# Optimization experiments

Measured on AMD Instinct MI355X. Metric: run time of the kernel, lower is better.

Reference implementation:

```python
import jax, jax.numpy as jnp
import numpy as np

B, T, D = 64, 256, 300
H = 256            # each_state = state_size // 2
G = 4 * H          # gate dim = state_size * 2
N = 8              # num_bases
M, KQ = 64, 64     # meta_dim, key_query_size
V = 10000          # meta vocab


def setup_inputs() -> dict:
    key = jax.random.key(0)
    ks = jax.random.split(key, 16)
    s = 0.05
    return {
        'x': jax.random.normal(ks[0], (B, T, D), jnp.float32),
        'length': jax.random.randint(ks[1], (B,), 1, T + 1),
        'user_idx': jax.random.randint(ks[2], (B,), 0, V),
        'item_idx': jax.random.randint(ks[3], (B,), 0, V),
        'user_emb': jax.random.normal(ks[4], (V, M), jnp.float32) * s,
        'item_emb': jax.random.normal(ks[5], (V, M), jnp.float32) * s,
        'W1': jax.random.normal(ks[6], (2 * M, KQ), jnp.float32) * s,
        'b1': jax.random.normal(ks[7], (KQ,), jnp.float32) * s,
        'W2': jax.random.normal(ks[8], (KQ, N), jnp.float32) * s,
        'Wih': jax.random.normal(ks[9], (N, G, D), jnp.float32) * s,
        'Whh': jax.random.normal(ks[10], (N, G, H), jnp.float32) * s,
        'bias': jax.random.normal(ks[11], (N, G), jnp.float32) * s,
        'Wih_r': jax.random.normal(ks[12], (N, G, D), jnp.float32) * s,
        'Whh_r': jax.random.normal(ks[13], (N, G, H), jnp.float32) * s,
        'bias_r': jax.random.normal(ks[14], (N, G), jnp.float32) * s,
    }


def _run_dir(xs, mask, Wi, Wh, bb):
    # xs: [T,B,D], mask: [T,B] True where state forced to zero
    b, h = xs.shape[1], Wh.shape[2]
    h0 = jnp.zeros((b, h), xs.dtype)

    def step(carry, inp):
        hx, cx = carry
        xt, m = inp
        gates = (jnp.einsum('bgi,bi->bg', Wi, xt)
                 + jnp.einsum('bgh,bh->bg', Wh, hx) + bb)
        ig, fg, gg, og = jnp.split(gates, 4, axis=1)
        cy = jax.nn.sigmoid(fg) * cx + jax.nn.sigmoid(ig) * jnp.tanh(gg)
        hy = jax.nn.sigmoid(og) * jnp.tanh(cy)
        cy = jnp.where(m[:, None], 0.0, cy)
        hy = jnp.where(m[:, None], 0.0, hy)
        return (hy, cy), hy

    _, hs = jax.lax.scan(step, (h0, h0), (xs, mask))
    return hs  # [T,B,H]


def reference(x, length, user_idx, item_idx, user_emb, item_emb,
              W1, b1, W2, Wih, Whh, bias, Wih_r, Whh_r, bias_r):
    # basis mixing coefficients per sample
    q = jnp.concatenate([user_emb[user_idx], item_emb[item_idx]], axis=1)  # [B,2M]
    c = jax.nn.softmax(jnp.tanh(q @ W1 + b1) @ W2, axis=1)                 # [B,N]
    mix = lambda w: jnp.einsum('bn,n...->b...', c, w)

    Bc, Tc = x.shape[0], x.shape[1]
    t = jnp.arange(Tc)
    mask_f = t[:, None] >= length[None, :]            # length - 1 < i
    mask_r = (Tc - t)[:, None] > length[None, :]      # maxlength - i > length

    xs = jnp.swapaxes(x, 0, 1)                        # [T,B,D]
    h_f = _run_dir(xs, mask_f, mix(Wih), mix(Whh), mix(bias))
    h_r = _run_dir(xs[::-1], mask_r, mix(Wih_r), mix(Whh_r), mix(bias_r))
    h_r = h_r[::-1]                                   # un-reverse in time
    return jnp.concatenate([h_f, h_r], axis=-1).swapaxes(0, 1)  # [B,T,2H]
```

## Files before the change

kernel.cpp:

```cpp
#include <hip/hip_runtime.h>

#define B_ 64
#define T_ 256
#define D_ 300
#define DP_ 320
#define H_ 256
#define G_ 1024
#define N_ 8

typedef unsigned int u32;
typedef unsigned short u16;
typedef __attribute__((ext_vector_type(8))) short short8;
typedef __attribute__((ext_vector_type(4))) float f32x4;
typedef __attribute__((ext_vector_type(4))) u32 u32x4;
typedef __attribute__((ext_vector_type(2))) u32 u32x2;
typedef _Float16 h2 __attribute__((ext_vector_type(2)));
typedef __fp16 fp16x2 __attribute__((ext_vector_type(2)));

__device__ __forceinline__ u16 f2bf(float f){
  union {float f; u32 u;} v; v.f = f;
  u32 r = (v.u + 0x7fffu + ((v.u>>16)&1u)) >> 16;
  return (u16)r;
}
__device__ __forceinline__ float bflo(u32 u){
  union {u32 u; float f;} v; v.u = u<<16; return v.f;
}
__device__ __forceinline__ float bfhi(u32 u){
  union {u32 u; float f;} v; v.u = u & 0xffff0000u; return v.f;
}
__device__ __forceinline__ float sigm(float x){ return 1.0f/(1.0f+__expf(-x)); }
__device__ __forceinline__ float tanh_(float x){ return 2.0f/(1.0f+__expf(-2.0f*x)) - 1.0f; }

__device__ __forceinline__ float fdot2(u32 a, u32 b, float c){
  union { u32 u; h2 h; } ua, ub; ua.u = a; ub.u = b;
#if __has_builtin(__builtin_amdgcn_fdot2)
  return __builtin_amdgcn_fdot2(ua.h, ub.h, c, false);
#else
  return c + (float)ua.h.x*(float)ub.h.x + (float)ua.h.y*(float)ub.h.y;
#endif
}
__device__ __forceinline__ u32 pkf16(float a, float b){
  union { fp16x2 h; u32 u; } v; v.h = __builtin_amdgcn_cvt_pkrtz(a, b); return v.u;
}

__global__ void __launch_bounds__(64) k_coef(
    const int* __restrict__ uidx, const int* __restrict__ iidx,
    const float* __restrict__ uemb, const float* __restrict__ iemb,
    const float* __restrict__ W1, const float* __restrict__ b1,
    const float* __restrict__ W2, float* __restrict__ coef)
{
  __shared__ float q[128];
  __shared__ float hid[64];
  __shared__ float lg[8];
  int b = blockIdx.x, t = threadIdx.x;
  int u = uidx[b], it = iidx[b];
  q[t]      = uemb[(size_t)u*64 + t];
  q[64 + t] = iemb[(size_t)it*64 + t];
  __syncthreads();
  float s = b1[t];
  for (int j = 0; j < 128; ++j) s = fmaf(q[j], W1[j*64 + t], s);
  hid[t] = tanhf(s);
  __syncthreads();
  if (t < 8) {
    float s2 = 0.f;
    for (int j = 0; j < 64; ++j) s2 = fmaf(hid[j], W2[j*8 + t], s2);
    lg[t] = s2;
  }
  __syncthreads();
  if (t == 0) {
    float mx = lg[0];
    for (int n = 1; n < 8; ++n) mx = fmaxf(mx, lg[n]);
    float e[8], den = 0.f;
    for (int n = 0; n < 8; ++n){ e[n] = __expf(lg[n]-mx); den += e[n]; }
    for (int n = 0; n < 8; ++n) coef[b*8+n] = e[n]/den;
  }
}

__global__ void __launch_bounds__(256) k_mix_whh(
    const float* __restrict__ Whh_f, const float* __restrict__ Whh_r,
    const float* __restrict__ bias_f, const float* __restrict__ bias_r,
    const float* __restrict__ coef, u32* __restrict__ blob, float* __restrict__ bias_m)
{
  int gblk = blockIdx.x;
  int dir  = blockIdx.y;
  int tid  = threadIdx.x;
  const float* Wsel = dir ? Whh_r : Whh_f;
  const float* bsel = dir ? bias_r : bias_f;
  __shared__ float bs[N_][8][H_];
  for (int v = 0; v < 64; ++v){
    int i = v*256 + tid;
    int n = i >> 11, gl = (i >> 8) & 7, c = i & 255;
    bs[n][gl][c] = Wsel[((size_t)n*G_ + gblk*8 + gl)*H_ + c];
  }
  __syncthreads();
  int t2l = tid & 7, ii = tid >> 3;
  int tid2 = gblk*8 + t2l;
  int gg = tid2 >> 2, q = tid2 & 3;
  int cidx = ii >> 2, e = ii & 3;
  int p = q*32 + ((cidx + 2*q)&7)*4 + e;
  int glbase = gg*4 - gblk*8;
  float bw0[4][8], bw1[4][8];
  #pragma unroll
  for (int l = 0; l < 4; ++l)
    #pragma unroll
    for (int n = 0; n < 8; ++n){
      bw0[l][n] = bs[n][glbase + l][2*p];
      bw1[l][n] = bs[n][glbase + l][2*p + 1];
    }
  for (int b = 0; b < B_; ++b){
    float c8[8];
    #pragma unroll
    for (int n = 0; n < 8; ++n) c8[n] = coef[b*8+n];
    u32x4 ov;
    #pragma unroll
    for (int l = 0; l < 4; ++l){
      float w0 = 0.f, w1 = 0.f;
      #pragma unroll
      for (int n = 0; n < 8; ++n){ w0 = fmaf(c8[n], bw0[l][n], w0); w1 = fmaf(c8[n], bw1[l][n], w1); }
      ov[l] = pkf16(w0, w1);
    }
    size_t chain = (size_t)(dir*B_ + b);
    *(u32x4*)(blob + ((chain*32 + ii)*1024 + tid2)*4) = ov;
    if (tid < 8){
      float bb = 0.f;
      #pragma unroll
      for (int n = 0; n < 8; ++n) bb = fmaf(c8[n], bsel[n*G_ + gblk*8 + tid], bb);
      bias_m[chain*G_ + gblk*8 + tid] = bb;
    }
  }
}

__global__ void __launch_bounds__(256) k_mix_wi(
    const float* __restrict__ Wih_f, const float* __restrict__ Wih_r,
    const float* __restrict__ coef, u32* __restrict__ WimU)
{
  int gblk = blockIdx.x;
  int dir  = blockIdx.y;
  int tid  = threadIdx.x;
  const float* Wsel = dir ? Wih_r : Wih_f;
  __shared__ float bs[N_][8][D_];
  for (int v = 0; v < 75; ++v){
    int i = v*256 + tid;
    int n = i/2400, rem = i%2400, gl = rem/300, c = rem%300;
    bs[n][gl][c] = Wsel[((size_t)n*G_ + gblk*8 + gl)*D_ + c];
  }
  __syncthreads();
  float bw[5][2][8];
  int rowv[5], cpv[5];
  #pragma unroll
  for (int v = 0; v < 5; ++v){
    int idx = v*256 + tid;
    int row = idx/160, cp = idx%160;
    rowv[v] = row; cpv[v] = cp;
    #pragma unroll
    for (int n = 0; n < 8; ++n){
      bw[v][0][n] = (cp < 150) ? bs[n][row][2*cp]   : 0.f;
      bw[v][1][n] = (cp < 150) ? bs[n][row][2*cp+1] : 0.f;
    }
  }
  for (int b = 0; b < B_; ++b){
    float c8[8];
    #pragma unroll
    for (int n = 0; n < 8; ++n) c8[n] = coef[b*8+n];
    #pragma unroll
    for (int v = 0; v < 5; ++v){
      float w0 = 0.f, w1 = 0.f;
      #pragma unroll
      for (int n = 0; n < 8; ++n){ w0 = fmaf(c8[n], bw[v][0][n], w0); w1 = fmaf(c8[n], bw[v][1][n], w1); }
      WimU[(((size_t)(dir*B_+b)*G_ + gblk*8 + rowv[v])*160) + cpv[v]] = (u32)f2bf(w0) | ((u32)f2bf(w1) << 16);
    }
  }
}

__global__ void __launch_bounds__(256) k_xpad(const float* __restrict__ x, u32* __restrict__ xpadU)
{
  int o = blockIdx.x*256 + threadIdx.x;
  int bt = o/160, cp = o%160;
  float v0 = (cp < 150) ? x[(size_t)bt*D_ + 2*cp]   : 0.f;
  float v1 = (cp < 150) ? x[(size_t)bt*D_ + 2*cp+1] : 0.f;
  xpadU[o] = (u32)f2bf(v0) | ((u32)f2bf(v1) << 16);
}

__global__ void __launch_bounds__(256,2) k_gemm(
    const u16* __restrict__ xpad, const u16* __restrict__ Wim,
    const float* __restrict__ bias_m, u16* __restrict__ xproj)
{
  int bx = blockIdx.x;
  int b  = blockIdx.y, dir = blockIdx.z;
  int tt = bx >> 3, tg = bx & 7;
  int tid = threadIdx.x;
  int wid = tid >> 6, lane = tid & 63;
  int wr = wid >> 1, wc = wid & 1;
  __shared__ u16 As[128][72];
  __shared__ u16 Bs[128][72];
  const u16* Ap = xpad + ((size_t)b*T_ + tt*128)*DP_;
  const u16* Bp = Wim + (((size_t)dir*B_ + b)*G_ + tg*128)*DP_;
  f32x4 acc[4][4];
  #pragma unroll
  for (int i = 0; i < 4; ++i)
    #pragma unroll
    for (int j = 0; j < 4; ++j) acc[i][j] = (f32x4){0.f,0.f,0.f,0.f};
  for (int kt = 0; kt < 5; ++kt){
    int k0 = kt*64;
    #pragma unroll
    for (int i = 0; i < 4; ++i){
      int ci = i*256 + tid;
      int row = ci >> 3, cc = (ci & 7)*8;
      *(u32x4*)&As[row][cc] = *(const u32x4*)(Ap + (size_t)row*DP_ + k0 + cc);
      *(u32x4*)&Bs[row][cc] = *(const u32x4*)(Bp + (size_t)row*DP_ + k0 + cc);
    }
    __syncthreads();
    #pragma unroll
    for (int kk = 0; kk < 2; ++kk){
      short8 af[4], bfr[4];
      #pragma unroll
      for (int mi = 0; mi < 4; ++mi) af[mi]  = *(const short8*)&As[wr*64 + mi*16 + (lane&15)][kk*32 + (lane>>4)*8];
      #pragma unroll
      for (int ni = 0; ni < 4; ++ni) bfr[ni] = *(const short8*)&Bs[wc*64 + ni*16 + (lane&15)][kk*32 + (lane>>4)*8];
      #pragma unroll
      for (int mi = 0; mi < 4; ++mi)
        #pragma unroll
        for (int ni = 0; ni < 4; ++ni)
          acc[mi][ni] = __builtin_amdgcn_mfma_f32_16x16x32_bf16(af[mi], bfr[ni], acc[mi][ni], 0,0,0);
    }
    __syncthreads();
  }
  int r4 = (lane >> 4)*4, cg = lane & 15;
  const float* bmp = bias_m + (size_t)(dir*B_ + b)*G_;
  #pragma unroll
  for (int ni = 0; ni < 4; ++ni){
    int g = tg*128 + wc*64 + ni*16 + cg;
    float bsv = bmp[g];
    #pragma unroll
    for (int mi = 0; mi < 4; ++mi)
      #pragma unroll
      for (int j = 0; j < 4; ++j){
        int t = tt*128 + wr*64 + mi*16 + r4 + j;
        xproj[(((size_t)dir*B_ + b)*T_ + t)*G_ + g] = f2bf(acc[mi][ni][j] + bsv);
      }
  }
}

__global__ void __launch_bounds__(1024) k_rec(
    const u32* __restrict__ blob, const u32* __restrict__ xprojU,
    const int* __restrict__ length, float* __restrict__ out)
{
  int chain = blockIdx.x;
  int dir = chain >> 6, b = chain & 63;
  int tid = threadIdx.x;
  int gg = tid >> 2, q = tid & 3;
  __shared__ u32 wlds[8][1024][4];
  __shared__ __align__(16) float gates4[256][4];
  __shared__ __align__(16) u16 hp16[256];
  const u32* hp32 = (const u32*)hp16;

  u32 w[96];
  const u32* bp = blob + (size_t)chain*32*1024*4;
  #pragma unroll
  for (int ii = 0; ii < 24; ++ii){
    u32x4 v = *(const u32x4*)(bp + ((size_t)ii*1024 + tid)*4);
    w[4*ii] = v.x; w[4*ii+1] = v.y; w[4*ii+2] = v.z; w[4*ii+3] = v.w;
  }
  #pragma unroll
  for (int ii = 24; ii < 32; ++ii){
    u32x4 v = *(const u32x4*)(bp + ((size_t)ii*1024 + tid)*4);
    *(u32x4*)&wlds[ii-24][tid][0] = v;
  }
  if (tid < 256) hp16[tid] = 0;
  int len = length[b];
  const u32* xp = xprojU + (size_t)chain*T_*512;
  float* outp = out + (size_t)b*T_*512 + dir*H_;
  float cst = 0.f;
  __syncthreads();

  for (int step = 0; step < len; ++step){
    int t = dir ? (len-1-step) : step;
    u32 xv0 = 0, xv1 = 0;
    if (q == 0){
      u32x2 xv = *(const u32x2*)(xp + (size_t)t*512 + 2*gg);
      xv0 = xv.x; xv1 = xv.y;
    }
    float a0 = 0.f, a1 = 0.f, a2 = 0.f, a3 = 0.f;
    #pragma unroll
    for (int cidx = 0; cidx < 8; ++cidx){
      int c4 = (cidx + 2*q) & 7;
      u32x4 hq = *(const u32x4*)&hp32[q*32 + c4*4];
      if (cidx < 6){
        #pragma unroll
        for (int e = 0; e < 4; ++e){
          u32 hv = hq[e];
          a0 = fdot2(w[cidx*16 + e*4 + 0], hv, a0);
          a1 = fdot2(w[cidx*16 + e*4 + 1], hv, a1);
          a2 = fdot2(w[cidx*16 + e*4 + 2], hv, a2);
          a3 = fdot2(w[cidx*16 + e*4 + 3], hv, a3);
        }
      } else {
        #pragma unroll
        for (int e = 0; e < 4; ++e){
          u32x4 wv = *(const u32x4*)&wlds[cidx*4 + e - 24][tid][0];
          u32 hv = hq[e];
          a0 = fdot2(wv.x, hv, a0);
          a1 = fdot2(wv.y, hv, a1);
          a2 = fdot2(wv.z, hv, a2);
          a3 = fdot2(wv.w, hv, a3);
        }
      }
    }
    a0 += __shfl_xor(a0, 1); a0 += __shfl_xor(a0, 2);
    a1 += __shfl_xor(a1, 1); a1 += __shfl_xor(a1, 2);
    a2 += __shfl_xor(a2, 1); a2 += __shfl_xor(a2, 2);
    a3 += __shfl_xor(a3, 1); a3 += __shfl_xor(a3, 2);
    if (q == 0){
      a0 += bflo(xv0); a1 += bfhi(xv0); a2 += bflo(xv1); a3 += bfhi(xv1);
      f32x4 g4; g4.x = a0; g4.y = a1; g4.z = a2; g4.w = a3;
      *(f32x4*)&gates4[gg][0] = g4;
    }
    __syncthreads();
    if (tid < 256){
      const float* gf = &gates4[0][0];
      float ig = gf[tid],       fg = gf[256 + tid];
      float g_ = gf[512 + tid], og = gf[768 + tid];
      float i_ = sigm(ig), f_ = sigm(fg), gt = tanh_(g_), o_ = sigm(og);
      float cn = fmaf(f_, cst, i_*gt);
      float hy = o_ * tanh_(cn);
      cst = cn;
      ((u16*)hp16)[tid] = (u16)(pkf16(hy, hy) & 0xffffu);
      outp[(size_t)t*512 + tid] = hy;
    }
    __syncthreads();
  }
}

extern "C" void kernel_launch(void* const* d_in, const int* in_sizes, int n_in,
                              void* d_out, int out_size, void* d_ws, size_t ws_size,
                              hipStream_t stream)
{
  const float* x      = (const float*)d_in[0];
  const int*   length = (const int*)d_in[1];
  const int*   uidx   = (const int*)d_in[2];
  const int*   iidx   = (const int*)d_in[3];
  const float* uemb   = (const float*)d_in[4];
  const float* iemb   = (const float*)d_in[5];
  const float* W1     = (const float*)d_in[6];
  const float* b1     = (const float*)d_in[7];
  const float* W2     = (const float*)d_in[8];
  const float* Wih    = (const float*)d_in[9];
  const float* Whh    = (const float*)d_in[10];
  const float* bias   = (const float*)d_in[11];
  const float* Wih_r  = (const float*)d_in[12];
  const float* Whh_r  = (const float*)d_in[13];
  const float* bias_r = (const float*)d_in[14];
  float* out = (float*)d_out;
  char* ws = (char*)d_ws;

  float* coef   = (float*)(ws + 0);
  float* bias_m = (float*)(ws + 2048);
  u32*   blob   = (u32*)  (ws + 526336);
  u16*   Wim    = (u16*)  (ws + 67635200);
  u16*   xpad   = (u16*)  (ws + 151521280);
  u16*   xproj  = (u16*)  (ws + 162007040);

  (void)hipMemsetAsync(d_out, 0, (size_t)out_size*sizeof(float), stream);
  if (ws_size < 229115904ull) return;

  hipLaunchKernelGGL(k_coef,    dim3(64),       dim3(64),   0, stream, uidx, iidx, uemb, iemb, W1, b1, W2, coef);
  hipLaunchKernelGGL(k_mix_whh, dim3(128,2),    dim3(256),  0, stream, Whh, Whh_r, bias, bias_r, coef, blob, bias_m);
  hipLaunchKernelGGL(k_mix_wi,  dim3(128,2),    dim3(256),  0, stream, Wih, Wih_r, coef, (u32*)Wim);
  hipLaunchKernelGGL(k_xpad,    dim3(10240),    dim3(256),  0, stream, x, (u32*)xpad);
  hipLaunchKernelGGL(k_gemm,    dim3(16,64,2),  dim3(256),  0, stream, xpad, Wim, bias_m, xproj);
  hipLaunchKernelGGL(k_rec,     dim3(128),      dim3(1024), 0, stream, blob, (const u32*)xproj, length, out);
}
```

Baseline: 623.3 us.

## Reorder gate rows per hidden unit to fuse LSTM cell and drop a barrier

The gate rows of the mixed recurrent weights and the input projection are permuted so that each quad of threads computes the i,f,g,o gates of one hidden unit. The cell update then runs directly in registers after the shuffle reduction, with no gate staging through shared memory. The hidden state is double-buffered, which leaves one barrier per time step instead of two. The projection is now stored as fp16 and added as the accumulator's initial value, which changes the rounding somewhat. All four lanes of a quad now compute the same nonlinearities redundantly.

```diff
diff --git a/kernel.cpp b/kernel.cpp
--- a/kernel.cpp
+++ b/kernel.cpp
@@ -28,6 +28,8 @@
 __device__ __forceinline__ float bfhi(u32 u){
   union {u32 u; float f;} v; v.u = u & 0xffff0000u; return v.f;
 }
+__device__ __forceinline__ float f16lo(u32 u){ union{u32 u; h2 h;} v; v.u=u; return (float)v.h.x; }
+__device__ __forceinline__ float f16hi(u32 u){ union{u32 u; h2 h;} v; v.u=u; return (float)v.h.y; }
 __device__ __forceinline__ float sigm(float x){ return 1.0f/(1.0f+__expf(-x)); }
 __device__ __forceinline__ float tanh_(float x){ return 2.0f/(1.0f+__expf(-2.0f*x)) - 1.0f; }
 
@@ -89,24 +91,27 @@
   __shared__ float bs[N_][8][H_];
   for (int v = 0; v < 64; ++v){
     int i = v*256 + tid;
-    int n = i >> 11, gl = (i >> 8) & 7, c = i & 255;
-    bs[n][gl][c] = Wsel[((size_t)n*G_ + gblk*8 + gl)*H_ + c];
+    int n = i >> 11, gl = (i >> 8) & 7, cc = i & 255;
+    int gate = (gl>>1)*256 + gblk*2 + (gl&1);
+    bs[n][gl][cc] = Wsel[((size_t)n*G_ + gate)*H_ + cc];
   }
   __syncthreads();
   int t2l = tid & 7, ii = tid >> 3;
   int tid2 = gblk*8 + t2l;
-  int gg = tid2 >> 2, q = tid2 & 3;
+  int q = tid2 & 3;
+  int clocal = (t2l >> 2) & 1;
   int cidx = ii >> 2, e = ii & 3;
   int p = q*32 + ((cidx + 2*q)&7)*4 + e;
-  int glbase = gg*4 - gblk*8;
   float bw0[4][8], bw1[4][8];
   #pragma unroll
-  for (int l = 0; l < 4; ++l)
+  for (int l = 0; l < 4; ++l){
+    int gl = l*2 + clocal;
     #pragma unroll
     for (int n = 0; n < 8; ++n){
-      bw0[l][n] = bs[n][glbase + l][2*p];
-      bw1[l][n] = bs[n][glbase + l][2*p + 1];
-    }
+      bw0[l][n] = bs[n][gl][2*p];
+      bw1[l][n] = bs[n][gl][2*p + 1];
+    }
+  }
   for (int b = 0; b < B_; ++b){
     float c8[8];
     #pragma unroll
@@ -183,7 +188,7 @@
 
 __global__ void __launch_bounds__(256,2) k_gemm(
     const u16* __restrict__ xpad, const u16* __restrict__ Wim,
-    const float* __restrict__ bias_m, u16* __restrict__ xproj)
+    const float* __restrict__ bias_m, u16* __restrict__ xq16)
 {
   int bx = blockIdx.x;
   int b  = blockIdx.y, dir = blockIdx.z;
@@ -227,32 +232,32 @@
   }
   int r4 = (lane >> 4)*4, cg = lane & 15;
   const float* bmp = bias_m + (size_t)(dir*B_ + b)*G_;
+  u16* xqp = xq16 + ((size_t)(dir*B_ + b)*T_)*1024;
   #pragma unroll
   for (int ni = 0; ni < 4; ++ni){
     int g = tg*128 + wc*64 + ni*16 + cg;
     float bsv = bmp[g];
+    int ci = g & 255, l = g >> 8;
     #pragma unroll
     for (int mi = 0; mi < 4; ++mi)
       #pragma unroll
       for (int j = 0; j < 4; ++j){
         int t = tt*128 + wr*64 + mi*16 + r4 + j;
-        xproj[(((size_t)dir*B_ + b)*T_ + t)*G_ + g] = f2bf(acc[mi][ni][j] + bsv);
+        xqp[(size_t)t*1024 + ci*4 + l] = (u16)pkf16(acc[mi][ni][j] + bsv, 0.f);
       }
   }
 }
 
 __global__ void __launch_bounds__(1024) k_rec(
-    const u32* __restrict__ blob, const u32* __restrict__ xprojU,
+    const u32* __restrict__ blob, const u32* __restrict__ xq,
     const int* __restrict__ length, float* __restrict__ out)
 {
   int chain = blockIdx.x;
   int dir = chain >> 6, b = chain & 63;
   int tid = threadIdx.x;
-  int gg = tid >> 2, q = tid & 3;
+  int c = tid >> 2, q = tid & 3;
   __shared__ u32 wlds[8][1024][4];
-  __shared__ __align__(16) float gates4[256][4];
-  __shared__ __align__(16) u16 hp16[256];
-  const u32* hp32 = (const u32*)hp16;
+  __shared__ __align__(16) u32 hpbuf[2][128];
 
   u32 w[96];
   const u32* bp = blob + (size_t)chain*32*1024*4;
@@ -266,10 +271,10 @@
     u32x4 v = *(const u32x4*)(bp + ((size_t)ii*1024 + tid)*4);
     *(u32x4*)&wlds[ii-24][tid][0] = v;
   }
-  if (tid < 256) hp16[tid] = 0;
+  if (tid < 128) hpbuf[0][tid] = 0u;
   int len = length[b];
-  const u32* xp = xprojU + (size_t)chain*T_*512;
-  float* outp = out + (size_t)b*T_*512 + dir*H_;
+  const u32* xp = xq + (size_t)chain*T_*512;
+  float* outp = out + (size_t)b*T_*512 + dir*H_ + c;
   float cst = 0.f;
   __syncthreads();
 
@@ -277,18 +282,19 @@
     int t = dir ? (len-1-step) : step;
     u32 xv0 = 0, xv1 = 0;
     if (q == 0){
-      u32x2 xv = *(const u32x2*)(xp + (size_t)t*512 + 2*gg);
+      u32x2 xv = *(const u32x2*)(xp + (size_t)t*512 + 2*c);
       xv0 = xv.x; xv1 = xv.y;
     }
-    float a0 = 0.f, a1 = 0.f, a2 = 0.f, a3 = 0.f;
+    const u32* hb = &hpbuf[step & 1][0];
+    float a0 = f16lo(xv0), a1 = f16hi(xv0), a2 = f16lo(xv1), a3 = f16hi(xv1);
     #pragma unroll
     for (int cidx = 0; cidx < 8; ++cidx){
       int c4 = (cidx + 2*q) & 7;
-      u32x4 hq = *(const u32x4*)&hp32[q*32 + c4*4];
+      u32x4 hqv = *(const u32x4*)&hb[q*32 + c4*4];
       if (cidx < 6){
         #pragma unroll
         for (int e = 0; e < 4; ++e){
-          u32 hv = hq[e];
+          u32 hv = hqv[e];
           a0 = fdot2(w[cidx*16 + e*4 + 0], hv, a0);
           a1 = fdot2(w[cidx*16 + e*4 + 1], hv, a1);
           a2 = fdot2(w[cidx*16 + e*4 + 2], hv, a2);
@@ -298,7 +304,7 @@
         #pragma unroll
         for (int e = 0; e < 4; ++e){
           u32x4 wv = *(const u32x4*)&wlds[cidx*4 + e - 24][tid][0];
-          u32 hv = hq[e];
+          u32 hv = hqv[e];
           a0 = fdot2(wv.x, hv, a0);
           a1 = fdot2(wv.y, hv, a1);
           a2 = fdot2(wv.z, hv, a2);
@@ -310,22 +316,13 @@
     a1 += __shfl_xor(a1, 1); a1 += __shfl_xor(a1, 2);
     a2 += __shfl_xor(a2, 1); a2 += __shfl_xor(a2, 2);
     a3 += __shfl_xor(a3, 1); a3 += __shfl_xor(a3, 2);
+    float i_ = sigm(a0), f_ = sigm(a1), gt = tanh_(a2), o_ = sigm(a3);
+    float cn = fmaf(f_, cst, i_*gt);
+    float hy = o_ * tanh_(cn);
+    cst = cn;
     if (q == 0){
-      a0 += bflo(xv0); a1 += bfhi(xv0); a2 += bflo(xv1); a3 += bfhi(xv1);
-      f32x4 g4; g4.x = a0; g4.y = a1; g4.z = a2; g4.w = a3;
-      *(f32x4*)&gates4[gg][0] = g4;
-    }
-    __syncthreads();
-    if (tid < 256){
-      const float* gf = &gates4[0][0];
-      float ig = gf[tid],       fg = gf[256 + tid];
-      float g_ = gf[512 + tid], og = gf[768 + tid];
-      float i_ = sigm(ig), f_ = sigm(fg), gt = tanh_(g_), o_ = sigm(og);
-      float cn = fmaf(f_, cst, i_*gt);
-      float hy = o_ * tanh_(cn);
-      cst = cn;
-      ((u16*)hp16)[tid] = (u16)(pkf16(hy, hy) & 0xffffu);
-      outp[(size_t)t*512 + tid] = hy;
+      ((u16*)&hpbuf[(step+1)&1][0])[c] = (u16)pkf16(hy, hy);
+      outp[(size_t)t*512] = hy;
     }
     __syncthreads();
   }
@@ -358,7 +355,7 @@
   u32*   blob   = (u32*)  (ws + 526336);
   u16*   Wim    = (u16*)  (ws + 67635200);
   u16*   xpad   = (u16*)  (ws + 151521280);
-  u16*   xproj  = (u16*)  (ws + 162007040);
+  u16*   xq16   = (u16*)  (ws + 162007040);
 
   (void)hipMemsetAsync(d_out, 0, (size_t)out_size*sizeof(float), stream);
   if (ws_size < 229115904ull) return;
@@ -367,6 +364,6 @@
   hipLaunchKernelGGL(k_mix_whh, dim3(128,2),    dim3(256),  0, stream, Whh, Whh_r, bias, bias_r, coef, blob, bias_m);
   hipLaunchKernelGGL(k_mix_wi,  dim3(128,2),    dim3(256),  0, stream, Wih, Wih_r, coef, (u32*)Wim);
   hipLaunchKernelGGL(k_xpad,    dim3(10240),    dim3(256),  0, stream, x, (u32*)xpad);
-  hipLaunchKernelGGL(k_gemm,    dim3(16,64,2),  dim3(256),  0, stream, xpad, Wim, bias_m, xproj);
-  hipLaunchKernelGGL(k_rec,     dim3(128),      dim3(1024), 0, stream, blob, (const u32*)xproj, length, out);
-}
+  hipLaunchKernelGGL(k_gemm,    dim3(16,64,2),  dim3(256),  0, stream, xpad, Wim, bias_m, xq16);
+  hipLaunchKernelGGL(k_rec,     dim3(128),      dim3(1024), 0, stream, blob, (const u32*)xq16, length, out);
+}
```

New measurement: 827.6 us. 32.8% more time.
